# Kernel tuning notes

Hardware: AMD Instinct MI355X
Metric: run time of the kernel (lower is better)

Reference implementation:

```python
import jax, jax.numpy as jnp
import numpy as np

B, N, L = 32, 1024, 128
K, D_E, H = 3, 16, 4


def setup_inputs() -> dict:
    key = jax.random.key(0)
    ks = jax.random.split(key, 7)
    return {
        "x": jax.random.normal(ks[0], (B, N, L), jnp.float32),
        # mild scaling on embeddings/projections keeps softmax logits in a sane range
        "psi_emb": jax.random.normal(ks[1], (N, D_E), jnp.float32) * 0.3,
        "psi": jnp.float32(1.0),
        "W_q": jax.random.normal(ks[2], (D_E, H, D_E), jnp.float32) * 0.2,
        "W_k": jax.random.normal(ks[3], (D_E, H, D_E), jnp.float32) * 0.2,
        "attn_alpha": jnp.float32(0.5),
        "F_w": jax.random.normal(ks[4], (H, D_E, K + 1, L), jnp.float32) * 0.1,
        "f_b": jax.random.normal(ks[5], (H, D_E), jnp.float32),
        "head_mix": jnp.ones((H,), jnp.float32),
    }


def reference(x, psi_emb, psi, W_q, W_k, attn_alpha, F_w, f_b, head_mix):
    # x: (B, N, L)
    n = x.shape[1]
    # --- gaussian adjacency: softmax over columns of exp(-psi * ||psi_i - psi_j||^2)
    diff = psi_emb[:, None, :] - psi_emb[None, :, :]          # (N, N, d_e)
    dist2 = jnp.sum(diff * diff, axis=-1)                     # (N, N)
    A_base = jax.nn.softmax(jnp.exp(-psi * dist2), axis=1)    # (N, N)
    # --- per-head attention adjacency
    Q = jnp.einsum('nd,dhm->nhm', psi_emb, W_q)               # (N, H, d_e)
    Kt = jnp.einsum('nd,dhm->nhm', psi_emb, W_k)              # (N, H, d_e)
    scale = 1.0 / jnp.sqrt(jnp.asarray(Q.shape[-1], x.dtype))
    A_attn = jax.nn.softmax(
        jnp.einsum('nhd,mhd->hnm', Q, Kt) * scale, axis=-1)   # (H, N, N)
    # --- sigmoid blend (all heads at once)
    alpha = jax.nn.sigmoid(attn_alpha)
    A_eff = alpha * A_base[None] + (1.0 - alpha) * A_attn     # (H, N, N)
    # --- Chebyshev recursion: T0 = I, T1 = A, Tk = 2 A T_{k-1} - T_{k-2}
    I = jnp.broadcast_to(jnp.eye(n, dtype=x.dtype), A_eff.shape)
    supports = [I, A_eff]
    for _ in range(2, K + 1):
        supports.append(2.0 * jnp.einsum('hnm,hml->hnl', A_eff, supports[-1]) - supports[-2])
    S = jnp.stack(supports, axis=1)                           # (H, K+1, N, N)
    # --- per-node filters
    W_filter = jnp.einsum('nd,hdkl->hnkl', psi_emb, F_w)      # (H, N, K+1, L)
    b_filter = jnp.einsum('nd,hd->hn', psi_emb, f_b)          # (H, N)
    # --- graph conv + node-specific contraction
    x_g = jnp.einsum('hknm,bml->bhknl', S, x)                 # (B, H, K+1, N, L)
    out_h = jnp.einsum('bhknl,hnkl->bhn', x_g, W_filter) + b_filter[None]
    # --- head mixing
    mix_w = jax.nn.softmax(head_mix, axis=0)                  # (H,)
    return jnp.einsum('bhn,h->bn', out_h, mix_w)              # (B, N)
```

## Files before the change

kernel.cpp:

```cpp
#include <hip/hip_runtime.h>
#include <cstdint>

#define NN 1024
#define BB 32
#define LL 128
#define DE 16
#define HH 4
#define K1 4
#define BD 512
#define NS 524288

using bf16x8 = __attribute__((ext_vector_type(8))) short;
using f32x4  = __attribute__((ext_vector_type(4))) float;
using u16x4  = __attribute__((ext_vector_type(4))) unsigned short;

__device__ inline unsigned short f2bf(float f) {
    unsigned u = __builtin_bit_cast(unsigned, f);
    u += 0x7FFFu + ((u >> 16) & 1u);
    return (unsigned short)(u >> 16);
}
__device__ inline float bf2f(unsigned short u) {
    return __builtin_bit_cast(float, (unsigned)u << 16);
}
__device__ inline ushort4 pk4(unsigned short a, unsigned short b,
                              unsigned short c, unsigned short d) {
    ushort4 t; t.x = a; t.y = b; t.z = c; t.w = d; return t;
}

typedef const __attribute__((address_space(1))) void gas_void;
typedef __attribute__((address_space(3))) void las_void;
#define GLD16(gsrc, ldst) \
    __builtin_amdgcn_global_load_lds((gas_void*)(gsrc), (las_void*)(ldst), 16, 0, 0)

struct LogitsSmem {
    float wqs[1024];
    float wks[1024];
    short EAj[64][56];
    short EBi[64][56];
    short KAj[64][136];
    short QBi[64][136];
    float nis[64];
    float njs[64];
    float part[4][5][64];
    short zblk[8];
};
struct XtSmem { float xs[64][128]; };

__global__ __launch_bounds__(256) void phase1(
    const float* __restrict__ psi_emb, const float* __restrict__ psi_p,
    const float* __restrict__ W_q, const float* __restrict__ W_k,
    const float* __restrict__ x, const float* __restrict__ F_w,
    short* __restrict__ bnt, short* __restrict__ ant, float* __restrict__ partials,
    short* __restrict__ xt, short* __restrict__ wtt, float* __restrict__ out)
{
    __shared__ __align__(16) char smem_raw[sizeof(LogitsSmem)];
    const int bid = blockIdx.x;
    const int tid = threadIdx.x;

    if (bid < 256) {
        LogitsSmem& S = *(LogitsSmem*)smem_raw;
        const int jb = bid & 15, ib = bid >> 4;
        const int i0 = ib * 64, j0 = jb * 64;

        *(float4*)&S.wqs[tid * 4] = *(const float4*)(W_q + tid * 4);
        *(float4*)&S.wks[tid * 4] = *(const float4*)(W_k + tid * 4);
        if (tid == 0) {
            const bf16x8 z = {0, 0, 0, 0, 0, 0, 0, 0};
            *(bf16x8*)&S.zblk[0] = z;
        }
        __syncthreads();

        {
            const int prow = tid >> 2, ph = tid & 3;
            float ei[DE], ej[DE];
            {
                const float* pei = psi_emb + (size_t)(i0 + prow) * DE;
                const float* pej = psi_emb + (size_t)(j0 + prow) * DE;
#pragma unroll
                for (int c = 0; c < 4; c++) {
                    const float4 vi = *(const float4*)(pei + c * 4);
                    ei[c * 4] = vi.x; ei[c * 4 + 1] = vi.y;
                    ei[c * 4 + 2] = vi.z; ei[c * 4 + 3] = vi.w;
                    const float4 vj = *(const float4*)(pej + c * 4);
                    ej[c * 4] = vj.x; ej[c * 4 + 1] = vj.y;
                    ej[c * 4 + 2] = vj.z; ej[c * 4 + 3] = vj.w;
                }
            }
            float qv[16], kv[16];
#pragma unroll
            for (int m = 0; m < 16; m++) { qv[m] = 0.f; kv[m] = 0.f; }
#pragma unroll
            for (int d = 0; d < DE; d++) {
                const float eid = ei[d], ejd = ej[d];
#pragma unroll
                for (int m = 0; m < 16; m++) {
                    qv[m] += eid * S.wqs[d * 64 + ph * 16 + m];
                    kv[m] += ejd * S.wks[d * 64 + ph * 16 + m];
                }
            }
            unsigned short qh[16], ql[16], kh[16], kl[16];
#pragma unroll
            for (int m = 0; m < 16; m++) {
                qh[m] = f2bf(qv[m]); ql[m] = f2bf(qv[m] - bf2f(qh[m]));
                kh[m] = f2bf(kv[m]); kl[m] = f2bf(kv[m] - bf2f(kh[m]));
            }
#pragma unroll
            for (int c = 0; c < 4; c++) {
                *(ushort4*)&S.QBi[prow][ph * 32 + c * 4] =
                    pk4(qh[c * 4], qh[c * 4 + 1], qh[c * 4 + 2], qh[c * 4 + 3]);
                *(ushort4*)&S.QBi[prow][ph * 32 + 16 + c * 4] =
                    pk4(ql[c * 4], ql[c * 4 + 1], ql[c * 4 + 2], ql[c * 4 + 3]);
                *(ushort4*)&S.KAj[prow][ph * 32 + c * 4] =
                    pk4(kh[c * 4], kh[c * 4 + 1], kh[c * 4 + 2], kh[c * 4 + 3]);
                *(ushort4*)&S.KAj[prow][ph * 32 + 16 + c * 4] =
                    pk4(kl[c * 4], kl[c * 4 + 1], kl[c * 4 + 2], kl[c * 4 + 3]);
            }
            if (ph == 0) {
                float ni = 0.f, nj = 0.f;
#pragma unroll
                for (int d = 0; d < DE; d++) { ni += ei[d] * ei[d]; nj += ej[d] * ej[d]; }
                S.nis[prow] = ni; S.njs[prow] = nj;
                unsigned short ih[16], il[16], jh[16], jl[16];
#pragma unroll
                for (int d = 0; d < DE; d++) {
                    ih[d] = f2bf(ei[d]); il[d] = f2bf(ei[d] - bf2f(ih[d]));
                    jh[d] = f2bf(ej[d]); jl[d] = f2bf(ej[d] - bf2f(jh[d]));
                }
#pragma unroll
                for (int c = 0; c < 4; c++) {
                    *(ushort4*)&S.EBi[prow][c * 4] =
                        pk4(ih[c * 4], ih[c * 4 + 1], ih[c * 4 + 2], ih[c * 4 + 3]);
                    *(ushort4*)&S.EBi[prow][16 + c * 4] =
                        pk4(il[c * 4], il[c * 4 + 1], il[c * 4 + 2], il[c * 4 + 3]);
                    *(ushort4*)&S.EAj[prow][c * 4] =
                        pk4(jh[c * 4], jh[c * 4 + 1], jh[c * 4 + 2], jh[c * 4 + 3]);
                    *(ushort4*)&S.EAj[prow][16 + c * 4] =
                        pk4(jl[c * 4], jl[c * 4 + 1], jl[c * 4 + 2], jl[c * 4 + 3]);
                }
            }
        }
        __syncthreads();

        const int w = tid >> 6, lane = tid & 63;
        const int q = lane >> 4, m16 = lane & 15;
        const float psi = psi_p[0];
        const short* zb = &S.zblk[0];

        {
            const bf16x8 aB = *(const bf16x8*)&S.EAj[w * 16 + m16][q * 8];
            f32x4 acc[4];
#pragma unroll
            for (int ct = 0; ct < 4; ct++) acc[ct] = (f32x4){0.f, 0.f, 0.f, 0.f};
#pragma unroll
            for (int ct = 0; ct < 4; ct++) {
                const short* bc = &S.EBi[ct * 16 + m16][0];
                const bf16x8 b1 = *(const bf16x8*)(bc + (q & 1) * 8);
                const bf16x8 b2 = *(const bf16x8*)(q < 2 ? bc + 16 + q * 8 : zb);
                acc[ct] = __builtin_amdgcn_mfma_f32_16x16x32_bf16(aB, b1, acc[ct], 0, 0, 0);
                acc[ct] = __builtin_amdgcn_mfma_f32_16x16x32_bf16(aB, b2, acc[ct], 0, 0, 0);
            }
            float njr[4];
#pragma unroll
            for (int r = 0; r < 4; r++) njr[r] = S.njs[w * 16 + q * 4 + r];
            const size_t tbase = (size_t)((j0 + w * 16 + q * 4) >> 3) * 8192 + (q & 1) * 4;
#pragma unroll
            for (int ct = 0; ct < 4; ct++) {
                const float nii = S.nis[ct * 16 + m16];
                float s = 0.f; unsigned short pw[4];
#pragma unroll
                for (int r = 0; r < 4; r++) {
                    const float d2 = nii + njr[r] - 2.f * acc[ct][r];
                    const float bn = __expf(__expf(-psi * d2));
                    s += bn; pw[r] = f2bf(bn);
                }
                *(ushort4*)(bnt + tbase + (size_t)(i0 + ct * 16 + m16) * 8) =
                    pk4(pw[0], pw[1], pw[2], pw[3]);
                s += __shfl_xor(s, 16, 64);
                s += __shfl_xor(s, 32, 64);
                if (q == 0) S.part[w][0][ct * 16 + m16] = s;
            }
        }
#pragma unroll
        for (int h = 0; h < HH; h++) {
            const bf16x8 aK = *(const bf16x8*)&S.KAj[w * 16 + m16][h * 32 + q * 8];
            f32x4 acc[4];
#pragma unroll
            for (int ct = 0; ct < 4; ct++) acc[ct] = (f32x4){0.f, 0.f, 0.f, 0.f};
#pragma unroll
            for (int ct = 0; ct < 4; ct++) {
                const short* qc = &S.QBi[ct * 16 + m16][h * 32];
                const bf16x8 b1 = *(const bf16x8*)(qc + (q & 1) * 8);
                const bf16x8 b2 = *(const bf16x8*)(q < 2 ? qc + 16 + q * 8 : zb);
                acc[ct] = __builtin_amdgcn_mfma_f32_16x16x32_bf16(aK, b1, acc[ct], 0, 0, 0);
                acc[ct] = __builtin_amdgcn_mfma_f32_16x16x32_bf16(aK, b2, acc[ct], 0, 0, 0);
            }
            const size_t tbase = (size_t)((j0 + w * 16 + q * 4) >> 3) * 8192 + (q & 1) * 4;
#pragma unroll
            for (int ct = 0; ct < 4; ct++) {
                float s = 0.f; unsigned short pw[4];
#pragma unroll
                for (int r = 0; r < 4; r++) {
                    const float an = __expf(acc[ct][r] * 0.25f);
                    s += an; pw[r] = f2bf(an);
                }
                *(ushort4*)(ant + (size_t)h * 1048576 + tbase +
                            (size_t)(i0 + ct * 16 + m16) * 8) =
                    pk4(pw[0], pw[1], pw[2], pw[3]);
                s += __shfl_xor(s, 16, 64);
                s += __shfl_xor(s, 32, 64);
                if (q == 0) S.part[w][1 + h][ct * 16 + m16] = s;
            }
        }
        __syncthreads();
        if (tid < 64) {
#pragma unroll
            for (int s = 0; s < 5; s++) {
                const float v = S.part[0][s][tid] + S.part[1][s][tid] +
                                S.part[2][s][tid] + S.part[3][s][tid];
                partials[(size_t)jb * 5120 + (size_t)s * 1024 + i0 + tid] = v;
            }
        }
    } else if (bid < 768) {
        XtSmem& X = *(XtSmem*)smem_raw;
        const int idx = bid - 256;
        const int m0 = (idx & 15) * 64;
        const int b  = idx >> 4;
        for (int i = tid; i < 2048; i += 256) {
            const int row = i >> 5, lq = i & 31;
            *(float4*)&X.xs[row][lq * 4] =
                *(const float4*)(x + ((size_t)(b * NN + m0 + row)) * LL + lq * 4);
        }
        __syncthreads();
        for (int j = tid; j < 1024; j += 256) {
            const int m = j & 63, lc = j >> 6;
            const float* s = &X.xs[m][lc * 8];
            uint4 pk;
            pk.x = f2bf(s[0]) | ((unsigned)f2bf(s[1]) << 16);
            pk.y = f2bf(s[2]) | ((unsigned)f2bf(s[3]) << 16);
            pk.z = f2bf(s[4]) | ((unsigned)f2bf(s[5]) << 16);
            pk.w = f2bf(s[6]) | ((unsigned)f2bf(s[7]) << 16);
            *(uint4*)(xt + (size_t)b * 131072 + (size_t)lc * 8192 + (size_t)(m0 + m) * 8) = pk;
        }
    } else if (bid < 784) {
        const int j = (bid - 768) * 256 + tid;
        const int lc = j >> 8, c = j & 255;
        const int h = c >> 6, k = (c >> 4) & 3, d = c & 15;
        const float* s = F_w + (size_t)((h * DE + d) * K1 + k) * LL + lc * 8;
        uint4 pk;
        pk.x = f2bf(s[0]) | ((unsigned)f2bf(s[1]) << 16);
        pk.y = f2bf(s[2]) | ((unsigned)f2bf(s[3]) << 16);
        pk.z = f2bf(s[4]) | ((unsigned)f2bf(s[5]) << 16);
        pk.w = f2bf(s[6]) | ((unsigned)f2bf(s[7]) << 16);
        *(uint4*)(wtt + (size_t)lc * 2048 + (size_t)c * 8) = pk;
    } else {
        const int idx = (bid - 784) * 256 + tid;
        const float4 z = {0.f, 0.f, 0.f, 0.f};
        *(float4*)(out + (size_t)idx * 8) = z;
        *(float4*)(out + (size_t)idx * 8 + 4) = z;
    }
}

__global__ __launch_bounds__(256) void phase2(
    const short* __restrict__ xt, const short* __restrict__ wtt,
    short* __restrict__ Gt,
    const short* __restrict__ bnt, const short* __restrict__ ant,
    const float* __restrict__ partials, const float* __restrict__ alpha_p,
    short* __restrict__ At)
{
    const int bid = blockIdx.x;
    const int tid = threadIdx.x;
    __shared__ float sums_l[5][64];

    if (bid < 1024) {
        const int cb = bid & 3;
        const int m0 = ((bid >> 2) & 15) * 64;
        const int bp = bid >> 6;
        const int wave = tid >> 6, lane = tid & 63;
        const int b  = bp * 2 + (wave >> 1);
        const int wc = wave & 1;
        const int q = lane >> 4, m16 = lane & 15;
        const short* xb = xt + (size_t)b * 131072;

        f32x4 acc[4][2];
#pragma unroll
        for (int mi = 0; mi < 4; mi++)
#pragma unroll
            for (int ni = 0; ni < 2; ni++) acc[mi][ni] = (f32x4){0.f, 0.f, 0.f, 0.f};

#pragma unroll
        for (int ks = 0; ks < 4; ks++) {
            const int kc = ks * 4 + q;
            bf16x8 a[4], bb[2];
#pragma unroll
            for (int mi = 0; mi < 4; mi++)
                a[mi] = *(const bf16x8*)(xb + (size_t)kc * 8192 + (size_t)(m0 + mi * 16 + m16) * 8);
#pragma unroll
            for (int ni = 0; ni < 2; ni++)
                bb[ni] = *(const bf16x8*)(wtt + (size_t)kc * 2048 +
                                          (size_t)(cb * 64 + wc * 32 + ni * 16 + m16) * 8);
#pragma unroll
            for (int mi = 0; mi < 4; mi++)
#pragma unroll
                for (int ni = 0; ni < 2; ni++)
                    acc[mi][ni] = __builtin_amdgcn_mfma_f32_16x16x32_bf16(a[mi], bb[ni], acc[mi][ni], 0, 0, 0);
        }

#pragma unroll
        for (int ni = 0; ni < 2; ni++) {
            const int cc = cb * 64 + wc * 32 + ni * 16 + m16;
            const int kk = (cc >> 4) & 3, hh = cc >> 6;
            const int col512 = b * 16 + (cc & 15);
            short* gdst = Gt + (size_t)(kk * 4 + hh) * 524288;
#pragma unroll
            for (int mi = 0; mi < 4; mi++) {
                const int row0 = m0 + mi * 16 + q * 4;
                ushort4 pk;
                pk.x = f2bf(acc[mi][ni][0]); pk.y = f2bf(acc[mi][ni][1]);
                pk.z = f2bf(acc[mi][ni][2]); pk.w = f2bf(acc[mi][ni][3]);
                *(ushort4*)(gdst + ((size_t)(row0 >> 3) * 512 + col512) * 8 + (row0 & 7)) = pk;
            }
        }
    } else {
        const int idx = bid - 1024;
        const int jb = idx & 15, ib = idx >> 4;
        const int i0 = ib * 64, j0 = jb * 64;
        const int lane = tid & 63, w = tid >> 6;
        {
            float acc = 0.f;
#pragma unroll
            for (int jb2 = 0; jb2 < 16; jb2++)
                acc += partials[(size_t)jb2 * 5120 + (size_t)w * 1024 + i0 + lane];
            sums_l[w][lane] = acc;
            if (w == 0) {
                float a4 = 0.f;
#pragma unroll
                for (int jb2 = 0; jb2 < 16; jb2++)
                    a4 += partials[(size_t)jb2 * 5120 + 4 * 1024 + i0 + lane];
                sums_l[4][lane] = a4;
            }
        }
        __syncthreads();
        const int i = lane, jg = w;
        const float alpha = 1.f / (1.f + __expf(-alpha_p[0]));
        const float ibs = alpha / sums_l[0][i];
        float ias[HH];
#pragma unroll
        for (int h = 0; h < HH; h++) ias[h] = (1.f - alpha) / sums_l[1 + h][i];

#pragma unroll
        for (int g = 0; g < 2; g++) {
            const size_t toff = (size_t)((j0 + jg * 16 + g * 8) >> 3) * 8192 + (size_t)(i0 + i) * 8;
            const uint4 bp = *(const uint4*)(bnt + toff);
            float bnv[8];
            bnv[0] = bf2f(bp.x & 0xFFFF); bnv[1] = bf2f(bp.x >> 16);
            bnv[2] = bf2f(bp.y & 0xFFFF); bnv[3] = bf2f(bp.y >> 16);
            bnv[4] = bf2f(bp.z & 0xFFFF); bnv[5] = bf2f(bp.z >> 16);
            bnv[6] = bf2f(bp.w & 0xFFFF); bnv[7] = bf2f(bp.w >> 16);
#pragma unroll
            for (int h = 0; h < HH; h++) {
                const uint4 ap = *(const uint4*)(ant + (size_t)h * 1048576 + toff);
                float av[8];
                av[0] = bf2f(ap.x & 0xFFFF); av[1] = bf2f(ap.x >> 16);
                av[2] = bf2f(ap.y & 0xFFFF); av[3] = bf2f(ap.y >> 16);
                av[4] = bf2f(ap.z & 0xFFFF); av[5] = bf2f(ap.z >> 16);
                av[6] = bf2f(ap.w & 0xFFFF); av[7] = bf2f(ap.w >> 16);
                unsigned short ow[8];
#pragma unroll
                for (int r = 0; r < 8; r++) ow[r] = f2bf(ibs * bnv[r] + ias[h] * av[r]);
                uint4 pk;
                pk.x = ow[0] | ((unsigned)ow[1] << 16);
                pk.y = ow[2] | ((unsigned)ow[3] << 16);
                pk.z = ow[4] | ((unsigned)ow[5] << 16);
                pk.w = ow[6] | ((unsigned)ow[7] << 16);
                *(uint4*)(At + (size_t)h * 1048576 + toff) = pk;
            }
        }
    }
}

__global__ __launch_bounds__(256) void gemm_mf(
    const short* __restrict__ At, const short* __restrict__ Bt,
    const short* __restrict__ Pt, const short* __restrict__ Qt,
    short* __restrict__ Ot, float scale, float pc, float qc)
{
    const int bid = blockIdx.x;
    const int h = (bid & 7) >> 1;
    const int tile = ((bid >> 3) << 1) | (bid & 1);
    const int c0 = (tile & 7) * 64;
    const int r0 = (tile >> 3) * 64;

    const short* Ah = At + (size_t)h * 1048576;
    const short* Bh = Bt + (size_t)h * 524288;
    const short* Ph = Pt + (size_t)h * 524288;
    const short* Qh = Qt + (size_t)h * 524288;
    short* Oh = Ot + (size_t)h * 524288;

    const int tid = threadIdx.x;
    const int wave = tid >> 6, lane = tid & 63;
    const int q = lane >> 4, m16 = lane & 15;
    const int wr = wave >> 1, wc = wave & 1;

    __shared__ __align__(16) short Asm[4][4][64][8];
    __shared__ __align__(16) short Bsm[4][4][64][8];

    const char* Abase = (const char*)Ah + (size_t)r0 * 16;
    const char* Bbase = (const char*)Bh + (size_t)c0 * 16;

#define STAGE_MF(itc, bufc)                                                     \
    do {                                                                        \
        const size_t ko_ = (size_t)((itc) * 4 + wave);                          \
        GLD16(Abase + ko_ * 16384 + (size_t)lane * 16, &Asm[bufc][wave][0][0]); \
        GLD16(Bbase + ko_ * 8192  + (size_t)lane * 16, &Bsm[bufc][wave][0][0]); \
    } while (0)

    f32x4 acc[2][2];
#pragma unroll
    for (int mi = 0; mi < 2; mi++)
#pragma unroll
        for (int ni = 0; ni < 2; ni++) acc[mi][ni] = (f32x4){0.f, 0.f, 0.f, 0.f};

    STAGE_MF(0, 0);
    STAGE_MF(1, 1);
    STAGE_MF(2, 2);

#pragma unroll
    for (int it = 0; it < 32; ++it) {
        if (it < 29) STAGE_MF(it + 3, (it + 3) & 3);
        if (it < 29)      asm volatile("s_waitcnt vmcnt(6)" ::: "memory");
        else if (it == 29) asm volatile("s_waitcnt vmcnt(4)" ::: "memory");
        else if (it == 30) asm volatile("s_waitcnt vmcnt(2)" ::: "memory");
        else               asm volatile("s_waitcnt vmcnt(0)" ::: "memory");
        __builtin_amdgcn_s_barrier();

        const int b = it & 3;
        const bf16x8 af0 = *(const bf16x8*)&Asm[b][q][wr * 32 + m16][0];
        const bf16x8 af1 = *(const bf16x8*)&Asm[b][q][wr * 32 + 16 + m16][0];
        const bf16x8 bf0 = *(const bf16x8*)&Bsm[b][q][wc * 32 + m16][0];
        const bf16x8 bf1 = *(const bf16x8*)&Bsm[b][q][wc * 32 + 16 + m16][0];
        acc[0][0] = __builtin_amdgcn_mfma_f32_16x16x32_bf16(af0, bf0, acc[0][0], 0, 0, 0);
        acc[0][1] = __builtin_amdgcn_mfma_f32_16x16x32_bf16(af0, bf1, acc[0][1], 0, 0, 0);
        acc[1][0] = __builtin_amdgcn_mfma_f32_16x16x32_bf16(af1, bf0, acc[1][0], 0, 0, 0);
        acc[1][1] = __builtin_amdgcn_mfma_f32_16x16x32_bf16(af1, bf1, acc[1][1], 0, 0, 0);

        __builtin_amdgcn_s_barrier();
    }
#undef STAGE_MF

#pragma unroll
    for (int mi = 0; mi < 2; mi++) {
        const int row0 = r0 + wr * 32 + mi * 16 + q * 4;
#pragma unroll
        for (int ni = 0; ni < 2; ni++) {
            const int cc = c0 + wc * 32 + ni * 16 + m16;
            const size_t off = ((size_t)(row0 >> 3) * 512 + cc) * 8 + (row0 & 7);
            const u16x4 pv = __builtin_nontemporal_load((const u16x4*)(Ph + off));
            float v[4];
            v[0] = scale * acc[mi][ni][0] + pc * bf2f(pv[0]);
            v[1] = scale * acc[mi][ni][1] + pc * bf2f(pv[1]);
            v[2] = scale * acc[mi][ni][2] + pc * bf2f(pv[2]);
            v[3] = scale * acc[mi][ni][3] + pc * bf2f(pv[3]);
            if (qc != 0.f) {
                const u16x4 qv = __builtin_nontemporal_load((const u16x4*)(Qh + off));
                v[0] += qc * bf2f(qv[0]); v[1] += qc * bf2f(qv[1]);
                v[2] += qc * bf2f(qv[2]); v[3] += qc * bf2f(qv[3]);
            }
            ushort4 pk;
            pk.x = f2bf(v[0]); pk.y = f2bf(v[1]); pk.z = f2bf(v[2]); pk.w = f2bf(v[3]);
            *(ushort4*)(Oh + off) = pk;
        }
    }
}

__global__ __launch_bounds__(256) void gemm3_out(
    const short* __restrict__ At, const short* __restrict__ Bt,
    const short* __restrict__ Pt, const short* __restrict__ Qt,
    const float* __restrict__ psi_emb, const float* __restrict__ f_b,
    const float* __restrict__ head_mix, float* __restrict__ out)
{
    const int bid = blockIdx.x;
    const int h = (bid & 7) >> 1;
    const int tile = ((bid >> 3) << 1) | (bid & 1);
    const int c0 = (tile & 7) * 64;
    const int r0 = (tile >> 3) * 64;

    const short* Ah = At + (size_t)h * 1048576;
    const short* Bh = Bt + (size_t)h * 524288;
    const short* Ph = Pt + (size_t)h * 524288;
    const short* Qh = Qt + (size_t)h * 524288;

    const int tid = threadIdx.x;
    const int wave = tid >> 6, lane = tid & 63;
    const int q = lane >> 4, m16 = lane & 15;
    const int wr = wave >> 1, wc = wave & 1;

    __shared__ float es[64][17];
    __shared__ __align__(16) short Asm[4][4][64][8];
    __shared__ __align__(16) short Bsm[4][4][64][8];

    {
        const int row = tid >> 2, dq = (tid & 3) * 4;
        const float4 ev = *(const float4*)(psi_emb + (size_t)(r0 + row) * DE + dq);
        es[row][dq] = ev.x; es[row][dq + 1] = ev.y;
        es[row][dq + 2] = ev.z; es[row][dq + 3] = ev.w;
    }
    __syncthreads();

    const char* Abase = (const char*)Ah + (size_t)r0 * 16;
    const char* Bbase = (const char*)Bh + (size_t)c0 * 16;

#define STAGE_G3(itc, bufc)                                                     \
    do {                                                                        \
        const size_t ko_ = (size_t)((itc) * 4 + wave);                          \
        GLD16(Abase + ko_ * 16384 + (size_t)lane * 16, &Asm[bufc][wave][0][0]); \
        GLD16(Bbase + ko_ * 8192  + (size_t)lane * 16, &Bsm[bufc][wave][0][0]); \
    } while (0)

    f32x4 acc[2][2];
#pragma unroll
    for (int mi = 0; mi < 2; mi++)
#pragma unroll
        for (int ni = 0; ni < 2; ni++) acc[mi][ni] = (f32x4){0.f, 0.f, 0.f, 0.f};

    STAGE_G3(0, 0);
    STAGE_G3(1, 1);
    STAGE_G3(2, 2);

#pragma unroll
    for (int it = 0; it < 32; ++it) {
        if (it < 29) STAGE_G3(it + 3, (it + 3) & 3);
        if (it < 29)      asm volatile("s_waitcnt vmcnt(6)" ::: "memory");
        else if (it == 29) asm volatile("s_waitcnt vmcnt(4)" ::: "memory");
        else if (it == 30) asm volatile("s_waitcnt vmcnt(2)" ::: "memory");
        else               asm volatile("s_waitcnt vmcnt(0)" ::: "memory");
        __builtin_amdgcn_s_barrier();

        const int b = it & 3;
        const bf16x8 af0 = *(const bf16x8*)&Asm[b][q][wr * 32 + m16][0];
        const bf16x8 af1 = *(const bf16x8*)&Asm[b][q][wr * 32 + 16 + m16][0];
        const bf16x8 bf0 = *(const bf16x8*)&Bsm[b][q][wc * 32 + m16][0];
        const bf16x8 bf1 = *(const bf16x8*)&Bsm[b][q][wc * 32 + 16 + m16][0];
        acc[0][0] = __builtin_amdgcn_mfma_f32_16x16x32_bf16(af0, bf0, acc[0][0], 0, 0, 0);
        acc[0][1] = __builtin_amdgcn_mfma_f32_16x16x32_bf16(af0, bf1, acc[0][1], 0, 0, 0);
        acc[1][0] = __builtin_amdgcn_mfma_f32_16x16x32_bf16(af1, bf0, acc[1][0], 0, 0, 0);
        acc[1][1] = __builtin_amdgcn_mfma_f32_16x16x32_bf16(af1, bf1, acc[1][1], 0, 0, 0);

        __builtin_amdgcn_s_barrier();
    }
#undef STAGE_G3

    const float hm0 = head_mix[0], hm1 = head_mix[1], hm2 = head_mix[2], hm3 = head_mix[3];
    const float mx = fmaxf(fmaxf(hm0, hm1), fmaxf(hm2, hm3));
    const float w0 = expf(hm0 - mx), w1 = expf(hm1 - mx), w2 = expf(hm2 - mx), w3 = expf(hm3 - mx);
    const float isum = 1.f / (w0 + w1 + w2 + w3);
    const float mwh = (h == 0 ? w0 : h == 1 ? w1 : h == 2 ? w2 : w3) * isum;
    const float fb = f_b[h * DE + m16];

#pragma unroll
    for (int mi = 0; mi < 2; mi++) {
        const int rloc0 = wr * 32 + mi * 16 + q * 4;
        const int row0 = r0 + rloc0;
#pragma unroll
        for (int ni = 0; ni < 2; ni++) {
            const int cc = c0 + wc * 32 + ni * 16 + m16;
            const int b = cc >> 4;
            const size_t off = ((size_t)(row0 >> 3) * 512 + cc) * 8 + (row0 & 7);
            const u16x4 pv = __builtin_nontemporal_load((const u16x4*)(Ph + off));
            const u16x4 qv = __builtin_nontemporal_load((const u16x4*)(Qh + off));
            float v[4];
            v[0] = acc[mi][ni][0] + bf2f(pv[0]) - bf2f(qv[0]);
            v[1] = acc[mi][ni][1] + bf2f(pv[1]) - bf2f(qv[1]);
            v[2] = acc[mi][ni][2] + bf2f(pv[2]) - bf2f(qv[2]);
            v[3] = acc[mi][ni][3] + bf2f(pv[3]) - bf2f(qv[3]);
#pragma unroll
            for (int r = 0; r < 4; r++) {
                float w = es[rloc0 + r][m16] * (v[r] + fb);
                w += __shfl_xor(w, 1, 64);
                w += __shfl_xor(w, 2, 64);
                w += __shfl_xor(w, 4, 64);
                w += __shfl_xor(w, 8, 64);
                if (m16 == 0)
                    atomicAdd(out + (size_t)b * NN + (row0 + r), mwh * w);
            }
        }
    }
}

extern "C" void kernel_launch(void* const* d_in, const int* in_sizes, int n_in,
                              void* d_out, int out_size, void* d_ws, size_t ws_size,
                              hipStream_t stream)
{
    const float* x          = (const float*)d_in[0];
    const float* psi_emb    = (const float*)d_in[1];
    const float* psi        = (const float*)d_in[2];
    const float* W_q        = (const float*)d_in[3];
    const float* W_k        = (const float*)d_in[4];
    const float* attn_alpha = (const float*)d_in[5];
    const float* F_w        = (const float*)d_in[6];
    const float* f_b        = (const float*)d_in[7];
    const float* head_mix   = (const float*)d_in[8];
    float* out = (float*)d_out;

    short* At  = (short*)d_ws;
    short* xt  = At + 4194304;
    short* wtt = xt + 4194304;
    short* Gt  = wtt + 32768;
    short* b2t = Gt + 8388608;
    short* b1t = b2t + 2097152;
    short* bnt = b1t + 2097152;
    short* ant = bnt + 1048576;
    float* partials = (float*)(ant + 4194304);

    const size_t need_bytes =
        (size_t)(4194304 + 4194304 + 32768 + 8388608 + 2097152 + 2097152 + 1048576 + 4194304) * 2 +
        (size_t)81920 * 4;
    if (ws_size < need_bytes) return;

    phase1<<<800, 256, 0, stream>>>(psi_emb, psi, W_q, W_k, x, F_w,
                                    bnt, ant, partials, xt, wtt, out);
    phase2<<<1280, 256, 0, stream>>>(xt, wtt, Gt, bnt, ant, partials,
                                     attn_alpha, At);

    gemm_mf<<<512, 256, 0, stream>>>(At, Gt + 12 * (size_t)524288, Gt + 8 * (size_t)524288,
                                     Gt , b2t, 2.f, 1.f, 0.f);
    gemm_mf<<<512, 256, 0, stream>>>(At, b2t, Gt + 4 * (size_t)524288,
                                     Gt + 12 * (size_t)524288, b1t, 2.f, 1.f, -1.f);
    gemm3_out<<<512, 256, 0, stream>>>(At, b1t, Gt, b2t, psi_emb, f_b, head_mix, out);
}
```

Baseline: 150.2 us.

## Fuse all phases into one cooperative persistent kernel with grid syncs

Merges the five separate launches (two prep phases and three Chebyshev GEMM stages) into one cooperative kernel of 512 blocks. Stages are separated by grid.sync instead of kernel boundaries, and each block now loops over twice the work where the old grids were larger. The goal is to remove launch gaps and tail effects between the short stages. The cost is grid-barrier overhead, occupancy capped at 2 blocks per CU, and less parallelism in stages that used to have 800 or 1280 blocks. A fallback path of five launches is kept in case the cooperative launch fails.

```diff
diff --git a/kernel.cpp b/kernel.cpp
--- a/kernel.cpp
+++ b/kernel.cpp
@@ -1,5 +1,8 @@
 #include <hip/hip_runtime.h>
+#include <hip/hip_cooperative_groups.h>
 #include <cstdint>
+
+namespace cg = cooperative_groups;
 
 #define NN 1024
 #define BB 32
@@ -44,346 +47,353 @@
     float part[4][5][64];
     short zblk[8];
 };
-struct XtSmem { float xs[64][128]; };
-
-__global__ __launch_bounds__(256) void phase1(
-    const float* __restrict__ psi_emb, const float* __restrict__ psi_p,
-    const float* __restrict__ W_q, const float* __restrict__ W_k,
-    const float* __restrict__ x, const float* __restrict__ F_w,
-    short* __restrict__ bnt, short* __restrict__ ant, float* __restrict__ partials,
-    short* __restrict__ xt, short* __restrict__ wtt, float* __restrict__ out)
-{
-    __shared__ __align__(16) char smem_raw[sizeof(LogitsSmem)];
-    const int bid = blockIdx.x;
-    const int tid = threadIdx.x;
-
-    if (bid < 256) {
-        LogitsSmem& S = *(LogitsSmem*)smem_raw;
-        const int jb = bid & 15, ib = bid >> 4;
-        const int i0 = ib * 64, j0 = jb * 64;
-
-        *(float4*)&S.wqs[tid * 4] = *(const float4*)(W_q + tid * 4);
-        *(float4*)&S.wks[tid * 4] = *(const float4*)(W_k + tid * 4);
-        if (tid == 0) {
-            const bf16x8 z = {0, 0, 0, 0, 0, 0, 0, 0};
-            *(bf16x8*)&S.zblk[0] = z;
-        }
-        __syncthreads();
-
+struct XtSmem   { float xs[64][128]; };
+struct BlendSmem{ float sums_l[5][64]; };
+struct GemmSmem {
+    short Asm[4][4][64][8];
+    short Bsm[4][4][64][8];
+    float es[64][17];
+};
+
+struct KArgs {
+    const float *x, *psi_emb, *psi, *W_q, *W_k, *attn_alpha, *F_w, *f_b, *head_mix;
+    float* out;
+    short *At, *xt, *wtt, *Gt, *b2t, *b1t, *bnt, *ant;
+    float* partials;
+};
+
+__device__ __forceinline__ void dev_logits(char* sm, const KArgs& A, int bid, int tid)
+{
+    LogitsSmem& S = *(LogitsSmem*)sm;
+    const int jb = bid & 15, ib = bid >> 4;
+    const int i0 = ib * 64, j0 = jb * 64;
+
+    *(float4*)&S.wqs[tid * 4] = *(const float4*)(A.W_q + tid * 4);
+    *(float4*)&S.wks[tid * 4] = *(const float4*)(A.W_k + tid * 4);
+    if (tid == 0) {
+        const bf16x8 z = {0, 0, 0, 0, 0, 0, 0, 0};
+        *(bf16x8*)&S.zblk[0] = z;
+    }
+    __syncthreads();
+
+    {
+        const int prow = tid >> 2, ph = tid & 3;
+        float ei[DE], ej[DE];
         {
-            const int prow = tid >> 2, ph = tid & 3;
-            float ei[DE], ej[DE];
-            {
-                const float* pei = psi_emb + (size_t)(i0 + prow) * DE;
-                const float* pej = psi_emb + (size_t)(j0 + prow) * DE;
-#pragma unroll
-                for (int c = 0; c < 4; c++) {
-                    const float4 vi = *(const float4*)(pei + c * 4);
-                    ei[c * 4] = vi.x; ei[c * 4 + 1] = vi.y;
-                    ei[c * 4 + 2] = vi.z; ei[c * 4 + 3] = vi.w;
-                    const float4 vj = *(const float4*)(pej + c * 4);
-                    ej[c * 4] = vj.x; ej[c * 4 + 1] = vj.y;
-                    ej[c * 4 + 2] = vj.z; ej[c * 4 + 3] = vj.w;
-                }
-            }
-            float qv[16], kv[16];
-#pragma unroll
-            for (int m = 0; m < 16; m++) { qv[m] = 0.f; kv[m] = 0.f; }
+            const float* pei = A.psi_emb + (size_t)(i0 + prow) * DE;
+            const float* pej = A.psi_emb + (size_t)(j0 + prow) * DE;
+#pragma unroll
+            for (int c = 0; c < 4; c++) {
+                const float4 vi = *(const float4*)(pei + c * 4);
+                ei[c * 4] = vi.x; ei[c * 4 + 1] = vi.y;
+                ei[c * 4 + 2] = vi.z; ei[c * 4 + 3] = vi.w;
+                const float4 vj = *(const float4*)(pej + c * 4);
+                ej[c * 4] = vj.x; ej[c * 4 + 1] = vj.y;
+                ej[c * 4 + 2] = vj.z; ej[c * 4 + 3] = vj.w;
+            }
+        }
+        float qv[16], kv[16];
+#pragma unroll
+        for (int m = 0; m < 16; m++) { qv[m] = 0.f; kv[m] = 0.f; }
+#pragma unroll
+        for (int d = 0; d < DE; d++) {
+            const float eid = ei[d], ejd = ej[d];
+#pragma unroll
+            for (int m = 0; m < 16; m++) {
+                qv[m] += eid * S.wqs[d * 64 + ph * 16 + m];
+                kv[m] += ejd * S.wks[d * 64 + ph * 16 + m];
+            }
+        }
+        unsigned short qh[16], ql[16], kh[16], kl[16];
+#pragma unroll
+        for (int m = 0; m < 16; m++) {
+            qh[m] = f2bf(qv[m]); ql[m] = f2bf(qv[m] - bf2f(qh[m]));
+            kh[m] = f2bf(kv[m]); kl[m] = f2bf(kv[m] - bf2f(kh[m]));
+        }
+#pragma unroll
+        for (int c = 0; c < 4; c++) {
+            *(ushort4*)&S.QBi[prow][ph * 32 + c * 4] =
+                pk4(qh[c * 4], qh[c * 4 + 1], qh[c * 4 + 2], qh[c * 4 + 3]);
+            *(ushort4*)&S.QBi[prow][ph * 32 + 16 + c * 4] =
+                pk4(ql[c * 4], ql[c * 4 + 1], ql[c * 4 + 2], ql[c * 4 + 3]);
+            *(ushort4*)&S.KAj[prow][ph * 32 + c * 4] =
+                pk4(kh[c * 4], kh[c * 4 + 1], kh[c * 4 + 2], kh[c * 4 + 3]);
+            *(ushort4*)&S.KAj[prow][ph * 32 + 16 + c * 4] =
+                pk4(kl[c * 4], kl[c * 4 + 1], kl[c * 4 + 2], kl[c * 4 + 3]);
+        }
+        if (ph == 0) {
+            float ni = 0.f, nj = 0.f;
+#pragma unroll
+            for (int d = 0; d < DE; d++) { ni += ei[d] * ei[d]; nj += ej[d] * ej[d]; }
+            S.nis[prow] = ni; S.njs[prow] = nj;
+            unsigned short ih[16], il[16], jh[16], jl[16];
 #pragma unroll
             for (int d = 0; d < DE; d++) {
-                const float eid = ei[d], ejd = ej[d];
-#pragma unroll
-                for (int m = 0; m < 16; m++) {
-                    qv[m] += eid * S.wqs[d * 64 + ph * 16 + m];
-                    kv[m] += ejd * S.wks[d * 64 + ph * 16 + m];
-                }
-            }
-            unsigned short qh[16], ql[16], kh[16], kl[16];
-#pragma unroll
-            for (int m = 0; m < 16; m++) {
-                qh[m] = f2bf(qv[m]); ql[m] = f2bf(qv[m] - bf2f(qh[m]));
-                kh[m] = f2bf(kv[m]); kl[m] = f2bf(kv[m] - bf2f(kh[m]));
+                ih[d] = f2bf(ei[d]); il[d] = f2bf(ei[d] - bf2f(ih[d]));
+                jh[d] = f2bf(ej[d]); jl[d] = f2bf(ej[d] - bf2f(jh[d]));
             }
 #pragma unroll
             for (int c = 0; c < 4; c++) {
-                *(ushort4*)&S.QBi[prow][ph * 32 + c * 4] =
-                    pk4(qh[c * 4], qh[c * 4 + 1], qh[c * 4 + 2], qh[c * 4 + 3]);
-                *(ushort4*)&S.QBi[prow][ph * 32 + 16 + c * 4] =
-                    pk4(ql[c * 4], ql[c * 4 + 1], ql[c * 4 + 2], ql[c * 4 + 3]);
-                *(ushort4*)&S.KAj[prow][ph * 32 + c * 4] =
-                    pk4(kh[c * 4], kh[c * 4 + 1], kh[c * 4 + 2], kh[c * 4 + 3]);
-                *(ushort4*)&S.KAj[prow][ph * 32 + 16 + c * 4] =
-                    pk4(kl[c * 4], kl[c * 4 + 1], kl[c * 4 + 2], kl[c * 4 + 3]);
-            }
-            if (ph == 0) {
-                float ni = 0.f, nj = 0.f;
-#pragma unroll
-                for (int d = 0; d < DE; d++) { ni += ei[d] * ei[d]; nj += ej[d] * ej[d]; }
-                S.nis[prow] = ni; S.njs[prow] = nj;
-                unsigned short ih[16], il[16], jh[16], jl[16];
-#pragma unroll
-                for (int d = 0; d < DE; d++) {
-                    ih[d] = f2bf(ei[d]); il[d] = f2bf(ei[d] - bf2f(ih[d]));
-                    jh[d] = f2bf(ej[d]); jl[d] = f2bf(ej[d] - bf2f(jh[d]));
-                }
-#pragma unroll
-                for (int c = 0; c < 4; c++) {
-                    *(ushort4*)&S.EBi[prow][c * 4] =
-                        pk4(ih[c * 4], ih[c * 4 + 1], ih[c * 4 + 2], ih[c * 4 + 3]);
-                    *(ushort4*)&S.EBi[prow][16 + c * 4] =
-                        pk4(il[c * 4], il[c * 4 + 1], il[c * 4 + 2], il[c * 4 + 3]);
-                    *(ushort4*)&S.EAj[prow][c * 4] =
-                        pk4(jh[c * 4], jh[c * 4 + 1], jh[c * 4 + 2], jh[c * 4 + 3]);
-                    *(ushort4*)&S.EAj[prow][16 + c * 4] =
-                        pk4(jl[c * 4], jl[c * 4 + 1], jl[c * 4 + 2], jl[c * 4 + 3]);
-                }
-            }
-        }
-        __syncthreads();
-
-        const int w = tid >> 6, lane = tid & 63;
-        const int q = lane >> 4, m16 = lane & 15;
-        const float psi = psi_p[0];
-        const short* zb = &S.zblk[0];
-
-        {
-            const bf16x8 aB = *(const bf16x8*)&S.EAj[w * 16 + m16][q * 8];
-            f32x4 acc[4];
-#pragma unroll
-            for (int ct = 0; ct < 4; ct++) acc[ct] = (f32x4){0.f, 0.f, 0.f, 0.f};
-#pragma unroll
-            for (int ct = 0; ct < 4; ct++) {
-                const short* bc = &S.EBi[ct * 16 + m16][0];
-                const bf16x8 b1 = *(const bf16x8*)(bc + (q & 1) * 8);
-                const bf16x8 b2 = *(const bf16x8*)(q < 2 ? bc + 16 + q * 8 : zb);
-                acc[ct] = __builtin_amdgcn_mfma_f32_16x16x32_bf16(aB, b1, acc[ct], 0, 0, 0);
-                acc[ct] = __builtin_amdgcn_mfma_f32_16x16x32_bf16(aB, b2, acc[ct], 0, 0, 0);
-            }
-            float njr[4];
-#pragma unroll
-            for (int r = 0; r < 4; r++) njr[r] = S.njs[w * 16 + q * 4 + r];
-            const size_t tbase = (size_t)((j0 + w * 16 + q * 4) >> 3) * 8192 + (q & 1) * 4;
-#pragma unroll
-            for (int ct = 0; ct < 4; ct++) {
-                const float nii = S.nis[ct * 16 + m16];
-                float s = 0.f; unsigned short pw[4];
-#pragma unroll
-                for (int r = 0; r < 4; r++) {
-                    const float d2 = nii + njr[r] - 2.f * acc[ct][r];
-                    const float bn = __expf(__expf(-psi * d2));
-                    s += bn; pw[r] = f2bf(bn);
-                }
-                *(ushort4*)(bnt + tbase + (size_t)(i0 + ct * 16 + m16) * 8) =
-                    pk4(pw[0], pw[1], pw[2], pw[3]);
-                s += __shfl_xor(s, 16, 64);
-                s += __shfl_xor(s, 32, 64);
-                if (q == 0) S.part[w][0][ct * 16 + m16] = s;
-            }
-        }
-#pragma unroll
-        for (int h = 0; h < HH; h++) {
-            const bf16x8 aK = *(const bf16x8*)&S.KAj[w * 16 + m16][h * 32 + q * 8];
-            f32x4 acc[4];
-#pragma unroll
-            for (int ct = 0; ct < 4; ct++) acc[ct] = (f32x4){0.f, 0.f, 0.f, 0.f};
-#pragma unroll
-            for (int ct = 0; ct < 4; ct++) {
-                const short* qc = &S.QBi[ct * 16 + m16][h * 32];
-                const bf16x8 b1 = *(const bf16x8*)(qc + (q & 1) * 8);
-                const bf16x8 b2 = *(const bf16x8*)(q < 2 ? qc + 16 + q * 8 : zb);
-                acc[ct] = __builtin_amdgcn_mfma_f32_16x16x32_bf16(aK, b1, acc[ct], 0, 0, 0);
-                acc[ct] = __builtin_amdgcn_mfma_f32_16x16x32_bf16(aK, b2, acc[ct], 0, 0, 0);
-            }
-            const size_t tbase = (size_t)((j0 + w * 16 + q * 4) >> 3) * 8192 + (q & 1) * 4;
-#pragma unroll
-            for (int ct = 0; ct < 4; ct++) {
-                float s = 0.f; unsigned short pw[4];
-#pragma unroll
-                for (int r = 0; r < 4; r++) {
-                    const float an = __expf(acc[ct][r] * 0.25f);
-                    s += an; pw[r] = f2bf(an);
-                }
-                *(ushort4*)(ant + (size_t)h * 1048576 + tbase +
-                            (size_t)(i0 + ct * 16 + m16) * 8) =
-                    pk4(pw[0], pw[1], pw[2], pw[3]);
-                s += __shfl_xor(s, 16, 64);
-                s += __shfl_xor(s, 32, 64);
-                if (q == 0) S.part[w][1 + h][ct * 16 + m16] = s;
-            }
-        }
-        __syncthreads();
-        if (tid < 64) {
-#pragma unroll
-            for (int s = 0; s < 5; s++) {
-                const float v = S.part[0][s][tid] + S.part[1][s][tid] +
-                                S.part[2][s][tid] + S.part[3][s][tid];
-                partials[(size_t)jb * 5120 + (size_t)s * 1024 + i0 + tid] = v;
-            }
-        }
-    } else if (bid < 768) {
-        XtSmem& X = *(XtSmem*)smem_raw;
-        const int idx = bid - 256;
-        const int m0 = (idx & 15) * 64;
-        const int b  = idx >> 4;
-        for (int i = tid; i < 2048; i += 256) {
-            const int row = i >> 5, lq = i & 31;
-            *(float4*)&X.xs[row][lq * 4] =
-                *(const float4*)(x + ((size_t)(b * NN + m0 + row)) * LL + lq * 4);
-        }
-        __syncthreads();
-        for (int j = tid; j < 1024; j += 256) {
-            const int m = j & 63, lc = j >> 6;
-            const float* s = &X.xs[m][lc * 8];
-            uint4 pk;
-            pk.x = f2bf(s[0]) | ((unsigned)f2bf(s[1]) << 16);
-            pk.y = f2bf(s[2]) | ((unsigned)f2bf(s[3]) << 16);
-            pk.z = f2bf(s[4]) | ((unsigned)f2bf(s[5]) << 16);
-            pk.w = f2bf(s[6]) | ((unsigned)f2bf(s[7]) << 16);
-            *(uint4*)(xt + (size_t)b * 131072 + (size_t)lc * 8192 + (size_t)(m0 + m) * 8) = pk;
-        }
-    } else if (bid < 784) {
-        const int j = (bid - 768) * 256 + tid;
-        const int lc = j >> 8, c = j & 255;
-        const int h = c >> 6, k = (c >> 4) & 3, d = c & 15;
-        const float* s = F_w + (size_t)((h * DE + d) * K1 + k) * LL + lc * 8;
+                *(ushort4*)&S.EBi[prow][c * 4] =
+                    pk4(ih[c * 4], ih[c * 4 + 1], ih[c * 4 + 2], ih[c * 4 + 3]);
+                *(ushort4*)&S.EBi[prow][16 + c * 4] =
+                    pk4(il[c * 4], il[c * 4 + 1], il[c * 4 + 2], il[c * 4 + 3]);
+                *(ushort4*)&S.EAj[prow][c * 4] =
+                    pk4(jh[c * 4], jh[c * 4 + 1], jh[c * 4 + 2], jh[c * 4 + 3]);
+                *(ushort4*)&S.EAj[prow][16 + c * 4] =
+                    pk4(jl[c * 4], jl[c * 4 + 1], jl[c * 4 + 2], jl[c * 4 + 3]);
+            }
+        }
+    }
+    __syncthreads();
+
+    const int w = tid >> 6, lane = tid & 63;
+    const int q = lane >> 4, m16 = lane & 15;
+    const float psi = A.psi[0];
+    const short* zb = &S.zblk[0];
+
+    {
+        const bf16x8 aB = *(const bf16x8*)&S.EAj[w * 16 + m16][q * 8];
+        f32x4 acc[4];
+#pragma unroll
+        for (int ct = 0; ct < 4; ct++) acc[ct] = (f32x4){0.f, 0.f, 0.f, 0.f};
+#pragma unroll
+        for (int ct = 0; ct < 4; ct++) {
+            const short* bc = &S.EBi[ct * 16 + m16][0];
+            const bf16x8 b1 = *(const bf16x8*)(bc + (q & 1) * 8);
+            const bf16x8 b2 = *(const bf16x8*)(q < 2 ? bc + 16 + q * 8 : zb);
+            acc[ct] = __builtin_amdgcn_mfma_f32_16x16x32_bf16(aB, b1, acc[ct], 0, 0, 0);
+            acc[ct] = __builtin_amdgcn_mfma_f32_16x16x32_bf16(aB, b2, acc[ct], 0, 0, 0);
+        }
+        float njr[4];
+#pragma unroll
+        for (int r = 0; r < 4; r++) njr[r] = S.njs[w * 16 + q * 4 + r];
+        const size_t tbase = (size_t)((j0 + w * 16 + q * 4) >> 3) * 8192 + (q & 1) * 4;
+#pragma unroll
+        for (int ct = 0; ct < 4; ct++) {
+            const float nii = S.nis[ct * 16 + m16];
+            float s = 0.f; unsigned short pw[4];
+#pragma unroll
+            for (int r = 0; r < 4; r++) {
+                const float d2 = nii + njr[r] - 2.f * acc[ct][r];
+                const float bn = __expf(__expf(-psi * d2));
+                s += bn; pw[r] = f2bf(bn);
+            }
+            *(ushort4*)(A.bnt + tbase + (size_t)(i0 + ct * 16 + m16) * 8) =
+                pk4(pw[0], pw[1], pw[2], pw[3]);
+            s += __shfl_xor(s, 16, 64);
+            s += __shfl_xor(s, 32, 64);
+            if (q == 0) S.part[w][0][ct * 16 + m16] = s;
+        }
+    }
+#pragma unroll
+    for (int h = 0; h < HH; h++) {
+        const bf16x8 aK = *(const bf16x8*)&S.KAj[w * 16 + m16][h * 32 + q * 8];
+        f32x4 acc[4];
+#pragma unroll
+        for (int ct = 0; ct < 4; ct++) acc[ct] = (f32x4){0.f, 0.f, 0.f, 0.f};
+#pragma unroll
+        for (int ct = 0; ct < 4; ct++) {
+            const short* qc = &S.QBi[ct * 16 + m16][h * 32];
+            const bf16x8 b1 = *(const bf16x8*)(qc + (q & 1) * 8);
+            const bf16x8 b2 = *(const bf16x8*)(q < 2 ? qc + 16 + q * 8 : zb);
+            acc[ct] = __builtin_amdgcn_mfma_f32_16x16x32_bf16(aK, b1, acc[ct], 0, 0, 0);
+            acc[ct] = __builtin_amdgcn_mfma_f32_16x16x32_bf16(aK, b2, acc[ct], 0, 0, 0);
+        }
+        const size_t tbase = (size_t)((j0 + w * 16 + q * 4) >> 3) * 8192 + (q & 1) * 4;
+#pragma unroll
+        for (int ct = 0; ct < 4; ct++) {
+            float s = 0.f; unsigned short pw[4];
+#pragma unroll
+            for (int r = 0; r < 4; r++) {
+                const float an = __expf(acc[ct][r] * 0.25f);
+                s += an; pw[r] = f2bf(an);
+            }
+            *(ushort4*)(A.ant + (size_t)h * 1048576 + tbase +
+                        (size_t)(i0 + ct * 16 + m16) * 8) =
+                pk4(pw[0], pw[1], pw[2], pw[3]);
+            s += __shfl_xor(s, 16, 64);
+            s += __shfl_xor(s, 32, 64);
+            if (q == 0) S.part[w][1 + h][ct * 16 + m16] = s;
+        }
+    }
+    __syncthreads();
+    if (tid < 64) {
+#pragma unroll
+        for (int s = 0; s < 5; s++) {
+            const float v = S.part[0][s][tid] + S.part[1][s][tid] +
+                            S.part[2][s][tid] + S.part[3][s][tid];
+            A.partials[(size_t)jb * 5120 + (size_t)s * 1024 + i0 + tid] = v;
+        }
+    }
+}
+
+__device__ __forceinline__ void dev_xt(char* sm, const float* __restrict__ x,
+                                       short* __restrict__ xt, int t, int tid)
+{
+    XtSmem& X = *(XtSmem*)sm;
+    const int m0 = (t & 15) * 64;
+    const int b  = t >> 4;
+    for (int i = tid; i < 2048; i += 256) {
+        const int row = i >> 5, lq = i & 31;
+        *(float4*)&X.xs[row][lq * 4] =
+            *(const float4*)(x + ((size_t)(b * NN + m0 + row)) * LL + lq * 4);
+    }
+    __syncthreads();
+    for (int j = tid; j < 1024; j += 256) {
+        const int m = j & 63, lc = j >> 6;
+        const float* s = &X.xs[m][lc * 8];
         uint4 pk;
         pk.x = f2bf(s[0]) | ((unsigned)f2bf(s[1]) << 16);
         pk.y = f2bf(s[2]) | ((unsigned)f2bf(s[3]) << 16);
         pk.z = f2bf(s[4]) | ((unsigned)f2bf(s[5]) << 16);
         pk.w = f2bf(s[6]) | ((unsigned)f2bf(s[7]) << 16);
-        *(uint4*)(wtt + (size_t)lc * 2048 + (size_t)c * 8) = pk;
-    } else {
-        const int idx = (bid - 784) * 256 + tid;
-        const float4 z = {0.f, 0.f, 0.f, 0.f};
-        *(float4*)(out + (size_t)idx * 8) = z;
-        *(float4*)(out + (size_t)idx * 8 + 4) = z;
-    }
-}
-
-__global__ __launch_bounds__(256) void phase2(
-    const short* __restrict__ xt, const short* __restrict__ wtt,
-    short* __restrict__ Gt,
-    const short* __restrict__ bnt, const short* __restrict__ ant,
-    const float* __restrict__ partials, const float* __restrict__ alpha_p,
-    short* __restrict__ At)
-{
-    const int bid = blockIdx.x;
-    const int tid = threadIdx.x;
-    __shared__ float sums_l[5][64];
-
-    if (bid < 1024) {
-        const int cb = bid & 3;
-        const int m0 = ((bid >> 2) & 15) * 64;
-        const int bp = bid >> 6;
-        const int wave = tid >> 6, lane = tid & 63;
-        const int b  = bp * 2 + (wave >> 1);
-        const int wc = wave & 1;
-        const int q = lane >> 4, m16 = lane & 15;
-        const short* xb = xt + (size_t)b * 131072;
-
-        f32x4 acc[4][2];
+        *(uint4*)(xt + (size_t)b * 131072 + (size_t)lc * 8192 + (size_t)(m0 + m) * 8) = pk;
+    }
+}
+
+__device__ __forceinline__ void dev_wtt(const float* __restrict__ F_w,
+                                        short* __restrict__ wtt, int w, int tid)
+{
+    const int j = w * 256 + tid;
+    const int lc = j >> 8, c = j & 255;
+    const int h = c >> 6, k = (c >> 4) & 3, d = c & 15;
+    const float* s = F_w + (size_t)((h * DE + d) * K1 + k) * LL + lc * 8;
+    uint4 pk;
+    pk.x = f2bf(s[0]) | ((unsigned)f2bf(s[1]) << 16);
+    pk.y = f2bf(s[2]) | ((unsigned)f2bf(s[3]) << 16);
+    pk.z = f2bf(s[4]) | ((unsigned)f2bf(s[5]) << 16);
+    pk.w = f2bf(s[6]) | ((unsigned)f2bf(s[7]) << 16);
+    *(uint4*)(wtt + (size_t)lc * 2048 + (size_t)c * 8) = pk;
+}
+
+__device__ __forceinline__ void dev_zero(float* __restrict__ out, int w, int tid)
+{
+    const int idx = w * 256 + tid;
+    const float4 z = {0.f, 0.f, 0.f, 0.f};
+    *(float4*)(out + (size_t)idx * 8) = z;
+    *(float4*)(out + (size_t)idx * 8 + 4) = z;
+}
+
+__device__ __forceinline__ void dev_gmfma(const short* __restrict__ xt,
+                                          const short* __restrict__ wtt,
+                                          short* __restrict__ Gt, int t, int tid)
+{
+    const int cb = t & 3;
+    const int m0 = ((t >> 2) & 15) * 64;
+    const int bp = t >> 6;
+    const int wave = tid >> 6, lane = tid & 63;
+    const int b  = bp * 2 + (wave >> 1);
+    const int wc = wave & 1;
+    const int q = lane >> 4, m16 = lane & 15;
+    const short* xb = xt + (size_t)b * 131072;
+
+    f32x4 acc[4][2];
+#pragma unroll
+    for (int mi = 0; mi < 4; mi++)
+#pragma unroll
+        for (int ni = 0; ni < 2; ni++) acc[mi][ni] = (f32x4){0.f, 0.f, 0.f, 0.f};
+
+#pragma unroll
+    for (int ks = 0; ks < 4; ks++) {
+        const int kc = ks * 4 + q;
+        bf16x8 a[4], bb[2];
 #pragma unroll
         for (int mi = 0; mi < 4; mi++)
-#pragma unroll
-            for (int ni = 0; ni < 2; ni++) acc[mi][ni] = (f32x4){0.f, 0.f, 0.f, 0.f};
-
-#pragma unroll
-        for (int ks = 0; ks < 4; ks++) {
-            const int kc = ks * 4 + q;
-            bf16x8 a[4], bb[2];
-#pragma unroll
-            for (int mi = 0; mi < 4; mi++)
-                a[mi] = *(const bf16x8*)(xb + (size_t)kc * 8192 + (size_t)(m0 + mi * 16 + m16) * 8);
+            a[mi] = *(const bf16x8*)(xb + (size_t)kc * 8192 + (size_t)(m0 + mi * 16 + m16) * 8);
+#pragma unroll
+        for (int ni = 0; ni < 2; ni++)
+            bb[ni] = *(const bf16x8*)(wtt + (size_t)kc * 2048 +
+                                      (size_t)(cb * 64 + wc * 32 + ni * 16 + m16) * 8);
+#pragma unroll
+        for (int mi = 0; mi < 4; mi++)
 #pragma unroll
             for (int ni = 0; ni < 2; ni++)
-                bb[ni] = *(const bf16x8*)(wtt + (size_t)kc * 2048 +
-                                          (size_t)(cb * 64 + wc * 32 + ni * 16 + m16) * 8);
-#pragma unroll
-            for (int mi = 0; mi < 4; mi++)
-#pragma unroll
-                for (int ni = 0; ni < 2; ni++)
-                    acc[mi][ni] = __builtin_amdgcn_mfma_f32_16x16x32_bf16(a[mi], bb[ni], acc[mi][ni], 0, 0, 0);
-        }
-
-#pragma unroll
-        for (int ni = 0; ni < 2; ni++) {
-            const int cc = cb * 64 + wc * 32 + ni * 16 + m16;
-            const int kk = (cc >> 4) & 3, hh = cc >> 6;
-            const int col512 = b * 16 + (cc & 15);
-            short* gdst = Gt + (size_t)(kk * 4 + hh) * 524288;
-#pragma unroll
-            for (int mi = 0; mi < 4; mi++) {
-                const int row0 = m0 + mi * 16 + q * 4;
-                ushort4 pk;
-                pk.x = f2bf(acc[mi][ni][0]); pk.y = f2bf(acc[mi][ni][1]);
-                pk.z = f2bf(acc[mi][ni][2]); pk.w = f2bf(acc[mi][ni][3]);
-                *(ushort4*)(gdst + ((size_t)(row0 >> 3) * 512 + col512) * 8 + (row0 & 7)) = pk;
-            }
-        }
-    } else {
-        const int idx = bid - 1024;
-        const int jb = idx & 15, ib = idx >> 4;
-        const int i0 = ib * 64, j0 = jb * 64;
-        const int lane = tid & 63, w = tid >> 6;
-        {
-            float acc = 0.f;
+                acc[mi][ni] = __builtin_amdgcn_mfma_f32_16x16x32_bf16(a[mi], bb[ni], acc[mi][ni], 0, 0, 0);
+    }
+
+#pragma unroll
+    for (int ni = 0; ni < 2; ni++) {
+        const int cc = cb * 64 + wc * 32 + ni * 16 + m16;
+        const int kk = (cc >> 4) & 3, hh = cc >> 6;
+        const int col512 = b * 16 + (cc & 15);
+        short* gdst = Gt + (size_t)(kk * 4 + hh) * 524288;
+#pragma unroll
+        for (int mi = 0; mi < 4; mi++) {
+            const int row0 = m0 + mi * 16 + q * 4;
+            ushort4 pk;
+            pk.x = f2bf(acc[mi][ni][0]); pk.y = f2bf(acc[mi][ni][1]);
+            pk.z = f2bf(acc[mi][ni][2]); pk.w = f2bf(acc[mi][ni][3]);
+            *(ushort4*)(gdst + ((size_t)(row0 >> 3) * 512 + col512) * 8 + (row0 & 7)) = pk;
+        }
+    }
+}
+
+__device__ __forceinline__ void dev_blend(char* sm, const KArgs& A, int idx, int tid)
+{
+    BlendSmem& BS = *(BlendSmem*)sm;
+    const int jb = idx & 15, ib = idx >> 4;
+    const int i0 = ib * 64, j0 = jb * 64;
+    const int lane = tid & 63, w = tid >> 6;
+    {
+        float acc = 0.f;
+#pragma unroll
+        for (int jb2 = 0; jb2 < 16; jb2++)
+            acc += A.partials[(size_t)jb2 * 5120 + (size_t)w * 1024 + i0 + lane];
+        BS.sums_l[w][lane] = acc;
+        if (w == 0) {
+            float a4 = 0.f;
 #pragma unroll
             for (int jb2 = 0; jb2 < 16; jb2++)
-                acc += partials[(size_t)jb2 * 5120 + (size_t)w * 1024 + i0 + lane];
-            sums_l[w][lane] = acc;
-            if (w == 0) {
-                float a4 = 0.f;
-#pragma unroll
-                for (int jb2 = 0; jb2 < 16; jb2++)
-                    a4 += partials[(size_t)jb2 * 5120 + 4 * 1024 + i0 + lane];
-                sums_l[4][lane] = a4;
-            }
-        }
-        __syncthreads();
-        const int i = lane, jg = w;
-        const float alpha = 1.f / (1.f + __expf(-alpha_p[0]));
-        const float ibs = alpha / sums_l[0][i];
-        float ias[HH];
-#pragma unroll
-        for (int h = 0; h < HH; h++) ias[h] = (1.f - alpha) / sums_l[1 + h][i];
-
-#pragma unroll
-        for (int g = 0; g < 2; g++) {
-            const size_t toff = (size_t)((j0 + jg * 16 + g * 8) >> 3) * 8192 + (size_t)(i0 + i) * 8;
-            const uint4 bp = *(const uint4*)(bnt + toff);
-            float bnv[8];
-            bnv[0] = bf2f(bp.x & 0xFFFF); bnv[1] = bf2f(bp.x >> 16);
-            bnv[2] = bf2f(bp.y & 0xFFFF); bnv[3] = bf2f(bp.y >> 16);
-            bnv[4] = bf2f(bp.z & 0xFFFF); bnv[5] = bf2f(bp.z >> 16);
-            bnv[6] = bf2f(bp.w & 0xFFFF); bnv[7] = bf2f(bp.w >> 16);
-#pragma unroll
-            for (int h = 0; h < HH; h++) {
-                const uint4 ap = *(const uint4*)(ant + (size_t)h * 1048576 + toff);
-                float av[8];
-                av[0] = bf2f(ap.x & 0xFFFF); av[1] = bf2f(ap.x >> 16);
-                av[2] = bf2f(ap.y & 0xFFFF); av[3] = bf2f(ap.y >> 16);
-                av[4] = bf2f(ap.z & 0xFFFF); av[5] = bf2f(ap.z >> 16);
-                av[6] = bf2f(ap.w & 0xFFFF); av[7] = bf2f(ap.w >> 16);
-                unsigned short ow[8];
-#pragma unroll
-                for (int r = 0; r < 8; r++) ow[r] = f2bf(ibs * bnv[r] + ias[h] * av[r]);
-                uint4 pk;
-                pk.x = ow[0] | ((unsigned)ow[1] << 16);
-                pk.y = ow[2] | ((unsigned)ow[3] << 16);
-                pk.z = ow[4] | ((unsigned)ow[5] << 16);
-                pk.w = ow[6] | ((unsigned)ow[7] << 16);
-                *(uint4*)(At + (size_t)h * 1048576 + toff) = pk;
-            }
-        }
-    }
-}
-
-__global__ __launch_bounds__(256) void gemm_mf(
+                a4 += A.partials[(size_t)jb2 * 5120 + 4 * 1024 + i0 + lane];
+            BS.sums_l[4][lane] = a4;
+        }
+    }
+    __syncthreads();
+    const int i = lane, jg = w;
+    const float alpha = 1.f / (1.f + __expf(-A.attn_alpha[0]));
+    const float ibs = alpha / BS.sums_l[0][i];
+    float ias[HH];
+#pragma unroll
+    for (int h = 0; h < HH; h++) ias[h] = (1.f - alpha) / BS.sums_l[1 + h][i];
+
+#pragma unroll
+    for (int g = 0; g < 2; g++) {
+        const size_t toff = (size_t)((j0 + jg * 16 + g * 8) >> 3) * 8192 + (size_t)(i0 + i) * 8;
+        const uint4 bp = *(const uint4*)(A.bnt + toff);
+        float bnv[8];
+        bnv[0] = bf2f(bp.x & 0xFFFF); bnv[1] = bf2f(bp.x >> 16);
+        bnv[2] = bf2f(bp.y & 0xFFFF); bnv[3] = bf2f(bp.y >> 16);
+        bnv[4] = bf2f(bp.z & 0xFFFF); bnv[5] = bf2f(bp.z >> 16);
+        bnv[6] = bf2f(bp.w & 0xFFFF); bnv[7] = bf2f(bp.w >> 16);
+#pragma unroll
+        for (int h = 0; h < HH; h++) {
+            const uint4 ap = *(const uint4*)(A.ant + (size_t)h * 1048576 + toff);
+            float av[8];
+            av[0] = bf2f(ap.x & 0xFFFF); av[1] = bf2f(ap.x >> 16);
+            av[2] = bf2f(ap.y & 0xFFFF); av[3] = bf2f(ap.y >> 16);
+            av[4] = bf2f(ap.z & 0xFFFF); av[5] = bf2f(ap.z >> 16);
+            av[6] = bf2f(ap.w & 0xFFFF); av[7] = bf2f(ap.w >> 16);
+            unsigned short ow[8];
+#pragma unroll
+            for (int r = 0; r < 8; r++) ow[r] = f2bf(ibs * bnv[r] + ias[h] * av[r]);
+            uint4 pk;
+            pk.x = ow[0] | ((unsigned)ow[1] << 16);
+            pk.y = ow[2] | ((unsigned)ow[3] << 16);
+            pk.z = ow[4] | ((unsigned)ow[5] << 16);
+            pk.w = ow[6] | ((unsigned)ow[7] << 16);
+            *(uint4*)(A.At + (size_t)h * 1048576 + toff) = pk;
+        }
+    }
+}
+
+template<bool USEQ>
+__device__ __forceinline__ void dev_gemm(char* sm,
     const short* __restrict__ At, const short* __restrict__ Bt,
     const short* __restrict__ Pt, const short* __restrict__ Qt,
-    short* __restrict__ Ot, float scale, float pc, float qc)
-{
-    const int bid = blockIdx.x;
+    short* __restrict__ Ot, float scale, float pc, float qc, int bid, int tid)
+{
+    GemmSmem& G = *(GemmSmem*)sm;
     const int h = (bid & 7) >> 1;
     const int tile = ((bid >> 3) << 1) | (bid & 1);
     const int c0 = (tile & 7) * 64;
@@ -392,25 +402,21 @@
     const short* Ah = At + (size_t)h * 1048576;
     const short* Bh = Bt + (size_t)h * 524288;
     const short* Ph = Pt + (size_t)h * 524288;
-    const short* Qh = Qt + (size_t)h * 524288;
+    const short* Qh = USEQ ? Qt + (size_t)h * 524288 : nullptr;
     short* Oh = Ot + (size_t)h * 524288;
 
-    const int tid = threadIdx.x;
     const int wave = tid >> 6, lane = tid & 63;
     const int q = lane >> 4, m16 = lane & 15;
     const int wr = wave >> 1, wc = wave & 1;
 
-    __shared__ __align__(16) short Asm[4][4][64][8];
-    __shared__ __align__(16) short Bsm[4][4][64][8];
-
     const char* Abase = (const char*)Ah + (size_t)r0 * 16;
     const char* Bbase = (const char*)Bh + (size_t)c0 * 16;
 
-#define STAGE_MF(itc, bufc)                                                     \
-    do {                                                                        \
-        const size_t ko_ = (size_t)((itc) * 4 + wave);                          \
-        GLD16(Abase + ko_ * 16384 + (size_t)lane * 16, &Asm[bufc][wave][0][0]); \
-        GLD16(Bbase + ko_ * 8192  + (size_t)lane * 16, &Bsm[bufc][wave][0][0]); \
+#define STAGE_X(itc, bufc)                                                        \
+    do {                                                                          \
+        const size_t ko_ = (size_t)((itc) * 4 + wave);                            \
+        GLD16(Abase + ko_ * 16384 + (size_t)lane * 16, &G.Asm[bufc][wave][0][0]); \
+        GLD16(Bbase + ko_ * 8192  + (size_t)lane * 16, &G.Bsm[bufc][wave][0][0]); \
     } while (0)
 
     f32x4 acc[2][2];
@@ -419,13 +425,13 @@
 #pragma unroll
         for (int ni = 0; ni < 2; ni++) acc[mi][ni] = (f32x4){0.f, 0.f, 0.f, 0.f};
 
-    STAGE_MF(0, 0);
-    STAGE_MF(1, 1);
-    STAGE_MF(2, 2);
+    STAGE_X(0, 0);
+    STAGE_X(1, 1);
+    STAGE_X(2, 2);
 
 #pragma unroll
     for (int it = 0; it < 32; ++it) {
-        if (it < 29) STAGE_MF(it + 3, (it + 3) & 3);
+        if (it < 29) STAGE_X(it + 3, (it + 3) & 3);
         if (it < 29)      asm volatile("s_waitcnt vmcnt(6)" ::: "memory");
         else if (it == 29) asm volatile("s_waitcnt vmcnt(4)" ::: "memory");
         else if (it == 30) asm volatile("s_waitcnt vmcnt(2)" ::: "memory");
@@ -433,10 +439,10 @@
         __builtin_amdgcn_s_barrier();
 
         const int b = it & 3;
-        const bf16x8 af0 = *(const bf16x8*)&Asm[b][q][wr * 32 + m16][0];
-        const bf16x8 af1 = *(const bf16x8*)&Asm[b][q][wr * 32 + 16 + m16][0];
-        const bf16x8 bf0 = *(const bf16x8*)&Bsm[b][q][wc * 32 + m16][0];
-        const bf16x8 bf1 = *(const bf16x8*)&Bsm[b][q][wc * 32 + 16 + m16][0];
+        const bf16x8 af0 = *(const bf16x8*)&G.Asm[b][q][wr * 32 + m16][0];
+        const bf16x8 af1 = *(const bf16x8*)&G.Asm[b][q][wr * 32 + 16 + m16][0];
+        const bf16x8 bf0 = *(const bf16x8*)&G.Bsm[b][q][wc * 32 + m16][0];
+        const bf16x8 bf1 = *(const bf16x8*)&G.Bsm[b][q][wc * 32 + 16 + m16][0];
         acc[0][0] = __builtin_amdgcn_mfma_f32_16x16x32_bf16(af0, bf0, acc[0][0], 0, 0, 0);
         acc[0][1] = __builtin_amdgcn_mfma_f32_16x16x32_bf16(af0, bf1, acc[0][1], 0, 0, 0);
         acc[1][0] = __builtin_amdgcn_mfma_f32_16x16x32_bf16(af1, bf0, acc[1][0], 0, 0, 0);
@@ -444,7 +450,7 @@
 
         __builtin_amdgcn_s_barrier();
     }
-#undef STAGE_MF
+#undef STAGE_X
 
 #pragma unroll
     for (int mi = 0; mi < 2; mi++) {
@@ -459,7 +465,7 @@
             v[1] = scale * acc[mi][ni][1] + pc * bf2f(pv[1]);
             v[2] = scale * acc[mi][ni][2] + pc * bf2f(pv[2]);
             v[3] = scale * acc[mi][ni][3] + pc * bf2f(pv[3]);
-            if (qc != 0.f) {
+            if (USEQ) {
                 const u16x4 qv = __builtin_nontemporal_load((const u16x4*)(Qh + off));
                 v[0] += qc * bf2f(qv[0]); v[1] += qc * bf2f(qv[1]);
                 v[2] += qc * bf2f(qv[2]); v[3] += qc * bf2f(qv[3]);
@@ -471,48 +477,39 @@
     }
 }
 
-__global__ __launch_bounds__(256) void gemm3_out(
-    const short* __restrict__ At, const short* __restrict__ Bt,
-    const short* __restrict__ Pt, const short* __restrict__ Qt,
-    const float* __restrict__ psi_emb, const float* __restrict__ f_b,
-    const float* __restrict__ head_mix, float* __restrict__ out)
-{
-    const int bid = blockIdx.x;
+__device__ __forceinline__ void dev_gemm3(char* sm, const KArgs& A, int bid, int tid)
+{
+    GemmSmem& G = *(GemmSmem*)sm;
     const int h = (bid & 7) >> 1;
     const int tile = ((bid >> 3) << 1) | (bid & 1);
     const int c0 = (tile & 7) * 64;
     const int r0 = (tile >> 3) * 64;
 
-    const short* Ah = At + (size_t)h * 1048576;
-    const short* Bh = Bt + (size_t)h * 524288;
-    const short* Ph = Pt + (size_t)h * 524288;
-    const short* Qh = Qt + (size_t)h * 524288;
-
-    const int tid = threadIdx.x;
+    const short* Ah = A.At  + (size_t)h * 1048576;
+    const short* Bh = A.b1t + (size_t)h * 524288;
+    const short* Ph = A.Gt  + (size_t)h * 524288;
+    const short* Qh = A.b2t + (size_t)h * 524288;
+
     const int wave = tid >> 6, lane = tid & 63;
     const int q = lane >> 4, m16 = lane & 15;
     const int wr = wave >> 1, wc = wave & 1;
 
-    __shared__ float es[64][17];
-    __shared__ __align__(16) short Asm[4][4][64][8];
-    __shared__ __align__(16) short Bsm[4][4][64][8];
-
     {
         const int row = tid >> 2, dq = (tid & 3) * 4;
-        const float4 ev = *(const float4*)(psi_emb + (size_t)(r0 + row) * DE + dq);
-        es[row][dq] = ev.x; es[row][dq + 1] = ev.y;
-        es[row][dq + 2] = ev.z; es[row][dq + 3] = ev.w;
+        const float4 ev = *(const float4*)(A.psi_emb + (size_t)(r0 + row) * DE + dq);
+        G.es[row][dq] = ev.x; G.es[row][dq + 1] = ev.y;
+        G.es[row][dq + 2] = ev.z; G.es[row][dq + 3] = ev.w;
     }
     __syncthreads();
 
     const char* Abase = (const char*)Ah + (size_t)r0 * 16;
     const char* Bbase = (const char*)Bh + (size_t)c0 * 16;
 
-#define STAGE_G3(itc, bufc)                                                     \
-    do {                                                                        \
-        const size_t ko_ = (size_t)((itc) * 4 + wave);                          \
-        GLD16(Abase + ko_ * 16384 + (size_t)lane * 16, &Asm[bufc][wave][0][0]); \
-        GLD16(Bbase + ko_ * 8192  + (size_t)lane * 16, &Bsm[bufc][wave][0][0]); \
+#define STAGE_Y(itc, bufc)                                                        \
+    do {                                                                          \
+        const size_t ko_ = (size_t)((itc) * 4 + wave);                            \
+        GLD16(Abase + ko_ * 16384 + (size_t)lane * 16, &G.Asm[bufc][wave][0][0]); \
+        GLD16(Bbase + ko_ * 8192  + (size_t)lane * 16, &G.Bsm[bufc][wave][0][0]); \
     } while (0)
 
     f32x4 acc[2][2];
@@ -521,13 +518,13 @@
 #pragma unroll
         for (int ni = 0; ni < 2; ni++) acc[mi][ni] = (f32x4){0.f, 0.f, 0.f, 0.f};
 
-    STAGE_G3(0, 0);
-    STAGE_G3(1, 1);
-    STAGE_G3(2, 2);
+    STAGE_Y(0, 0);
+    STAGE_Y(1, 1);
+    STAGE_Y(2, 2);
 
 #pragma unroll
     for (int it = 0; it < 32; ++it) {
-        if (it < 29) STAGE_G3(it + 3, (it + 3) & 3);
+        if (it < 29) STAGE_Y(it + 3, (it + 3) & 3);
         if (it < 29)      asm volatile("s_waitcnt vmcnt(6)" ::: "memory");
         else if (it == 29) asm volatile("s_waitcnt vmcnt(4)" ::: "memory");
         else if (it == 30) asm volatile("s_waitcnt vmcnt(2)" ::: "memory");
@@ -535,10 +532,10 @@
         __builtin_amdgcn_s_barrier();
 
         const int b = it & 3;
-        const bf16x8 af0 = *(const bf16x8*)&Asm[b][q][wr * 32 + m16][0];
-        const bf16x8 af1 = *(const bf16x8*)&Asm[b][q][wr * 32 + 16 + m16][0];
-        const bf16x8 bf0 = *(const bf16x8*)&Bsm[b][q][wc * 32 + m16][0];
-        const bf16x8 bf1 = *(const bf16x8*)&Bsm[b][q][wc * 32 + 16 + m16][0];
+        const bf16x8 af0 = *(const bf16x8*)&G.Asm[b][q][wr * 32 + m16][0];
+        const bf16x8 af1 = *(const bf16x8*)&G.Asm[b][q][wr * 32 + 16 + m16][0];
+        const bf16x8 bf0 = *(const bf16x8*)&G.Bsm[b][q][wc * 32 + m16][0];
+        const bf16x8 bf1 = *(const bf16x8*)&G.Bsm[b][q][wc * 32 + 16 + m16][0];
         acc[0][0] = __builtin_amdgcn_mfma_f32_16x16x32_bf16(af0, bf0, acc[0][0], 0, 0, 0);
         acc[0][1] = __builtin_amdgcn_mfma_f32_16x16x32_bf16(af0, bf1, acc[0][1], 0, 0, 0);
         acc[1][0] = __builtin_amdgcn_mfma_f32_16x16x32_bf16(af1, bf0, acc[1][0], 0, 0, 0);
@@ -546,14 +543,16 @@
 
         __builtin_amdgcn_s_barrier();
     }
-#undef STAGE_G3
-
-    const float hm0 = head_mix[0], hm1 = head_mix[1], hm2 = head_mix[2], hm3 = head_mix[3];
+#undef STAGE_Y
+
+    const float hm0 = A.head_mix[0], hm1 = A.head_mix[1],
+                hm2 = A.head_mix[2], hm3 = A.head_mix[3];
     const float mx = fmaxf(fmaxf(hm0, hm1), fmaxf(hm2, hm3));
-    const float w0 = expf(hm0 - mx), w1 = expf(hm1 - mx), w2 = expf(hm2 - mx), w3 = expf(hm3 - mx);
+    const float w0 = expf(hm0 - mx), w1 = expf(hm1 - mx),
+                w2 = expf(hm2 - mx), w3 = expf(hm3 - mx);
     const float isum = 1.f / (w0 + w1 + w2 + w3);
     const float mwh = (h == 0 ? w0 : h == 1 ? w1 : h == 2 ? w2 : w3) * isum;
-    const float fb = f_b[h * DE + m16];
+    const float fb = A.f_b[h * DE + m16];
 
 #pragma unroll
     for (int mi = 0; mi < 2; mi++) {
@@ -573,56 +572,120 @@
             v[3] = acc[mi][ni][3] + bf2f(pv[3]) - bf2f(qv[3]);
 #pragma unroll
             for (int r = 0; r < 4; r++) {
-                float w = es[rloc0 + r][m16] * (v[r] + fb);
+                float w = G.es[rloc0 + r][m16] * (v[r] + fb);
                 w += __shfl_xor(w, 1, 64);
                 w += __shfl_xor(w, 2, 64);
                 w += __shfl_xor(w, 4, 64);
                 w += __shfl_xor(w, 8, 64);
                 if (m16 == 0)
-                    atomicAdd(out + (size_t)b * NN + (row0 + r), mwh * w);
-            }
-        }
-    }
+                    atomicAdd(A.out + (size_t)b * NN + (row0 + r), mwh * w);
+            }
+        }
+    }
+}
+
+__device__ __forceinline__ void body_s0(char* sm, const KArgs& A, int bid, int tid)
+{
+    if (bid < 256) {
+        dev_logits(sm, A, bid, tid);
+    } else {
+        const int i = bid - 256;
+        dev_xt(sm, A.x, A.xt, i, tid);
+        __syncthreads();
+        dev_xt(sm, A.x, A.xt, i + 256, tid);
+        if (i < 16) dev_wtt(A.F_w, A.wtt, i, tid);
+        else if (i < 32) dev_zero(A.out, i - 16, tid);
+    }
+}
+__device__ __forceinline__ void body_s1(char* sm, const KArgs& A, int bid, int tid)
+{
+    dev_gmfma(A.xt, A.wtt, A.Gt, bid, tid);
+    dev_gmfma(A.xt, A.wtt, A.Gt, bid + 512, tid);
+    if (bid < 256) dev_blend(sm, A, bid, tid);
+}
+
+__global__ __launch_bounds__(256, 2) void kfused(KArgs A)
+{
+    __shared__ __align__(16) char sm[sizeof(LogitsSmem)];
+    cg::grid_group grid = cg::this_grid();
+    const int bid = blockIdx.x, tid = threadIdx.x;
+
+    body_s0(sm, A, bid, tid);
+    grid.sync();
+    body_s1(sm, A, bid, tid);
+    grid.sync();
+    dev_gemm<false>(sm, A.At, A.Gt + 12 * (size_t)NS, A.Gt + 8 * (size_t)NS,
+                    nullptr, A.b2t, 2.f, 1.f, 0.f, bid, tid);
+    grid.sync();
+    dev_gemm<true>(sm, A.At, A.b2t, A.Gt + 4 * (size_t)NS,
+                   A.Gt + 12 * (size_t)NS, A.b1t, 2.f, 1.f, -1.f, bid, tid);
+    grid.sync();
+    dev_gemm3(sm, A, bid, tid);
+}
+
+__global__ __launch_bounds__(256, 2) void w_s0(KArgs A) {
+    __shared__ __align__(16) char sm[sizeof(LogitsSmem)];
+    body_s0(sm, A, blockIdx.x, threadIdx.x);
+}
+__global__ __launch_bounds__(256, 2) void w_s1(KArgs A) {
+    __shared__ __align__(16) char sm[sizeof(LogitsSmem)];
+    body_s1(sm, A, blockIdx.x, threadIdx.x);
+}
+__global__ __launch_bounds__(256, 2) void w_g1(KArgs A) {
+    __shared__ __align__(16) char sm[sizeof(GemmSmem)];
+    dev_gemm<false>(sm, A.At, A.Gt + 12 * (size_t)NS, A.Gt + 8 * (size_t)NS,
+                    nullptr, A.b2t, 2.f, 1.f, 0.f, blockIdx.x, threadIdx.x);
+}
+__global__ __launch_bounds__(256, 2) void w_g2(KArgs A) {
+    __shared__ __align__(16) char sm[sizeof(GemmSmem)];
+    dev_gemm<true>(sm, A.At, A.b2t, A.Gt + 4 * (size_t)NS,
+                   A.Gt + 12 * (size_t)NS, A.b1t, 2.f, 1.f, -1.f,
+                   blockIdx.x, threadIdx.x);
+}
+__global__ __launch_bounds__(256, 2) void w_g3(KArgs A) {
+    __shared__ __align__(16) char sm[sizeof(GemmSmem)];
+    dev_gemm3(sm, A, blockIdx.x, threadIdx.x);
 }
 
 extern "C" void kernel_launch(void* const* d_in, const int* in_sizes, int n_in,
                               void* d_out, int out_size, void* d_ws, size_t ws_size,
                               hipStream_t stream)
 {
-    const float* x          = (const float*)d_in[0];
-    const float* psi_emb    = (const float*)d_in[1];
-    const float* psi        = (const float*)d_in[2];
-    const float* W_q        = (const float*)d_in[3];
-    const float* W_k        = (const float*)d_in[4];
-    const float* attn_alpha = (const float*)d_in[5];
-    const float* F_w        = (const float*)d_in[6];
-    const float* f_b        = (const float*)d_in[7];
-    const float* head_mix   = (const float*)d_in[8];
-    float* out = (float*)d_out;
-
-    short* At  = (short*)d_ws;
-    short* xt  = At + 4194304;
-    short* wtt = xt + 4194304;
-    short* Gt  = wtt + 32768;
-    short* b2t = Gt + 8388608;
-    short* b1t = b2t + 2097152;
-    short* bnt = b1t + 2097152;
-    short* ant = bnt + 1048576;
-    float* partials = (float*)(ant + 4194304);
+    KArgs A;
+    A.x          = (const float*)d_in[0];
+    A.psi_emb    = (const float*)d_in[1];
+    A.psi        = (const float*)d_in[2];
+    A.W_q        = (const float*)d_in[3];
+    A.W_k        = (const float*)d_in[4];
+    A.attn_alpha = (const float*)d_in[5];
+    A.F_w        = (const float*)d_in[6];
+    A.f_b        = (const float*)d_in[7];
+    A.head_mix   = (const float*)d_in[8];
+    A.out        = (float*)d_out;
+
+    A.At  = (short*)d_ws;
+    A.xt  = A.At + 4194304;
+    A.wtt = A.xt + 4194304;
+    A.Gt  = A.wtt + 32768;
+    A.b2t = A.Gt + 8388608;
+    A.b1t = A.b2t + 2097152;
+    A.bnt = A.b1t + 2097152;
+    A.ant = A.bnt + 1048576;
+    A.partials = (float*)(A.ant + 4194304);
 
     const size_t need_bytes =
         (size_t)(4194304 + 4194304 + 32768 + 8388608 + 2097152 + 2097152 + 1048576 + 4194304) * 2 +
         (size_t)81920 * 4;
     if (ws_size < need_bytes) return;
 
-    phase1<<<800, 256, 0, stream>>>(psi_emb, psi, W_q, W_k, x, F_w,
-                                    bnt, ant, partials, xt, wtt, out);
-    phase2<<<1280, 256, 0, stream>>>(xt, wtt, Gt, bnt, ant, partials,
-                                     attn_alpha, At);
-
-    gemm_mf<<<512, 256, 0, stream>>>(At, Gt + 12 * (size_t)524288, Gt + 8 * (size_t)524288,
-                                     Gt , b2t, 2.f, 1.f, 0.f);
-    gemm_mf<<<512, 256, 0, stream>>>(At, b2t, Gt + 4 * (size_t)524288,
-                                     Gt + 12 * (size_t)524288, b1t, 2.f, 1.f, -1.f);
-    gemm3_out<<<512, 256, 0, stream>>>(At, b1t, Gt, b2t, psi_emb, f_b, head_mix, out);
-}
+    void* params[] = { (void*)&A };
+    const hipError_t err = hipLaunchCooperativeKernel(
+        reinterpret_cast<void*>(kfused), dim3(512), dim3(256), params, 0, stream);
+    if (err != hipSuccess) {
+        w_s0<<<512, 256, 0, stream>>>(A);
+        w_s1<<<512, 256, 0, stream>>>(A);
+        w_g1<<<512, 256, 0, stream>>>(A);
+        w_g2<<<512, 256, 0, stream>>>(A);
+        w_g3<<<512, 256, 0, stream>>>(A);
+    }
+}
```

Result: slower. 386.5 us (+157.3%).
